# Kernel optimization log

Hardware: AMD Instinct MI355X
Metric: run time of the kernel (lower is better)

## Reference

```python
import jax, jax.numpy as jnp
import numpy as np
from jax import lax

V = 25          # skeleton joints
GAMMA = 9       # temporal kernel size
PAD = (GAMMA - 1) // 2
# (C_in, C_out, temporal_stride) for the 10 SpatialTemporalConv blocks
CHANNELS = [(3, 64, 1), (64, 64, 1), (64, 64, 1), (64, 64, 1),
            (64, 128, 2), (128, 128, 1), (128, 128, 1),
            (128, 256, 2), (256, 256, 1), (256, 256, 1)]


def setup_inputs() -> dict:
    key = jax.random.key(0)
    keys = jax.random.split(key, 1 + 2 * len(CHANNELS))
    N, T = 64, 300
    x = jax.random.normal(keys[0], (N, T, V, 3), jnp.float32)

    # Normalized adjacency (uni-labeling strategy): D^-1/2 (A + I) D^-1/2
    rng = np.random.default_rng(0)
    adj = (rng.random((V, V)) < 0.15).astype(np.float32)
    adj = np.maximum(adj, adj.T)
    adj = adj + np.eye(V, dtype=np.float32)
    dinv = 1.0 / np.sqrt(adj.sum(axis=1))
    A = jnp.asarray(dinv[:, None] * adj * dinv[None, :])

    inp = {"x": x, "A": A}
    for i, (cin, cout, _s) in enumerate(CHANNELS):
        inp[f"ws{i}"] = jax.random.normal(keys[1 + 2 * i], (cout, cin), jnp.float32) * np.float32(np.sqrt(2.0 / (cin * V)))
        inp[f"wt{i}"] = jax.random.normal(keys[2 + 2 * i], (cout, cout, GAMMA), jnp.float32) * np.float32(np.sqrt(2.0 / (cout * GAMMA)))
    return inp


def _st_block(f, A, ws, wt, stride):
    """One SpatialTemporalConv: 1x1 spatial GCN (channel mix + adjacency matmul),
    ReLU, then (gamma x 1) temporal conv with given stride, ReLU.
    f: (N, C_in, T, V) -> (N, C_out, T//stride, V)"""
    g = jnp.einsum('nctv,oc->notv', f, ws)       # 1x1 conv channel mixing
    g = jnp.einsum('nctv,vw->nctw', g, A)        # graph adjacency multiply
    g = jax.nn.relu(g)
    out = lax.conv_general_dilated(
        g, wt[:, :, :, None],                    # (O, I, gamma, 1)
        window_strides=(stride, 1),
        padding=((PAD, PAD), (0, 0)),
        dimension_numbers=('NCHW', 'OIHW', 'NCHW'))
    return jax.nn.relu(out)


def reference(x, A, ws0, ws1, ws2, ws3, ws4, ws5, ws6, ws7, ws8, ws9,
              wt0, wt1, wt2, wt3, wt4, wt5, wt6, wt7, wt8, wt9):
    ws = [ws0, ws1, ws2, ws3, ws4, ws5, ws6, ws7, ws8, ws9]
    wt = [wt0, wt1, wt2, wt3, wt4, wt5, wt6, wt7, wt8, wt9]
    f = jnp.transpose(x, (0, 3, 1, 2))  # (N,T,V,C) -> (N,C,T,V)
    for i, (_cin, _cout, s) in enumerate(CHANNELS):
        f = _st_block(f, A, ws[i], wt[i], s)
    return f  # (N, 256, T//4, V)
```

## Files before the change

### kernel.cpp

```cpp
#include <hip/hip_runtime.h>
#include <cstdint>

typedef unsigned short u16;
typedef unsigned int u32;
typedef __attribute__((ext_vector_type(8))) short short8v;
typedef __attribute__((ext_vector_type(4))) float float4v;

#define MFMA16 __builtin_amdgcn_mfma_f32_16x16x32_bf16

__device__ __forceinline__ u16 f2bf(float x) {
    union { float f; u32 u; } c; c.f = x;
    return (u16)((c.u + 0x7FFFu + ((c.u >> 16) & 1u)) >> 16);
}
__device__ __forceinline__ float bf2f(u16 h) {
    union { u32 u; float f; } c; c.u = ((u32)h) << 16;
    return c.f;
}

__device__ __forceinline__ void dma16(const void* g, void* l) {
    __builtin_amdgcn_global_load_lds(
        (const __attribute__((address_space(1))) u32*)g,
        (__attribute__((address_space(3))) u32*)l, 16, 0, 0);
}

__global__ void zinit(u32* p) { p[threadIdx.x] = 0u; }

__global__ __launch_bounds__(256)
void prep_w(const float* __restrict__ W, u16* __restrict__ dst,
            int M, int cin, int nIC, int TAPS, int total)
{
    int e = blockIdx.x * 256 + threadIdx.x;
    if (e >= total) return;
    int tmp = e;
    int j = tmp & 7; tmp >>= 3;
    int m = tmp % M; tmp /= M;
    int kg = tmp & 3; tmp >>= 2;
    int p = tmp & 1; tmp >>= 1;
    int ic = tmp % nIC;
    int tap = tmp / nIC;
    int i = ic * 32 + kg * 8 + j;
    float val = (i < cin) ? W[((size_t)m * cin + i) * TAPS + tap] : 0.f;
    u16 h = f2bf(val);
    dst[e] = p ? f2bf(val - bf2f(h)) : h;
}

__global__ __launch_bounds__(256)
void adj0(const float* __restrict__ x, const float* __restrict__ Am,
          u16* __restrict__ dstb, long dst_nstride, int dst_poff)
{
    __shared__ float A_s[25][26];
    for (int i2 = threadIdx.x; i2 < 625; i2 += 256) A_s[i2 / 25][i2 % 25] = Am[i2];
    __syncthreads();
    int t = blockIdx.x * 256 + threadIdx.x;
    int nl = blockIdx.y;
    if (t >= 300) return;
    const float* xp = x + ((size_t)nl * 300 + t) * 75;
    float acc[25][3];
#pragma unroll
    for (int w = 0; w < 25; ++w) { acc[w][0] = 0.f; acc[w][1] = 0.f; acc[w][2] = 0.f; }
    for (int v = 0; v < 25; ++v) {
        float x0 = xp[v * 3 + 0], x1 = xp[v * 3 + 1], x2 = xp[v * 3 + 2];
#pragma unroll
        for (int w = 0; w < 25; ++w) {
            float a = A_s[v][w];
            acc[w][0] = fmaf(a, x0, acc[w][0]);
            acc[w][1] = fmaf(a, x1, acc[w][1]);
            acc[w][2] = fmaf(a, x2, acc[w][2]);
        }
    }
    u16* dhi = dstb + (size_t)nl * dst_nstride;
    u16* dlo = dhi + dst_poff;
#pragma unroll
    for (int w = 0; w < 25; ++w) {
        u16 hb[32], lb[32];
#pragma unroll
        for (int c = 0; c < 32; ++c) { hb[c] = 0; lb[c] = 0; }
#pragma unroll
        for (int c = 0; c < 3; ++c) {
            float y = acc[w][c];
            u16 h = f2bf(y);
            hb[c] = h; lb[c] = f2bf(y - bf2f(h));
        }
        size_t o = ((size_t)w * 300 + t) * 32;
#pragma unroll
        for (int q = 0; q < 4; ++q) {
            *(uint4*)&dhi[o + q * 8] = *(const uint4*)&hb[q * 8];
            *(uint4*)&dlo[o + q * 8] = *(const uint4*)&lb[q * 8];
        }
    }
}

__global__ __launch_bounds__(256)
void adj_ip(u16* fb, const float* __restrict__ Am, int C, int Tin,
            long nstride, int poff)
{
    __shared__ float A_s[25][26];
    for (int i2 = threadIdx.x; i2 < 625; i2 += 256) A_s[i2 / 25][i2 % 25] = Am[i2];
    __syncthreads();
    const int C4 = C >> 2;
    int idx = blockIdx.x * 256 + threadIdx.x;
    if (idx >= Tin * C4) return;
    int t = idx / C4;
    int c = (idx - t * C4) * 4;
    u16* hi = fb + (size_t)blockIdx.y * nstride;
    u16* lo = hi + poff;
    float a0[25], a1[25], a2[25], a3[25];
#pragma unroll
    for (int w = 0; w < 25; ++w) { a0[w] = 0.f; a1[w] = 0.f; a2[w] = 0.f; a3[w] = 0.f; }
    for (int v = 0; v < 25; ++v) {
        size_t o = (size_t)(v * Tin + t) * C + c;
        ushort4 h4 = *(const ushort4*)&hi[o];
        ushort4 l4 = *(const ushort4*)&lo[o];
        float y0 = bf2f(h4.x) + bf2f(l4.x);
        float y1 = bf2f(h4.y) + bf2f(l4.y);
        float y2 = bf2f(h4.z) + bf2f(l4.z);
        float y3 = bf2f(h4.w) + bf2f(l4.w);
#pragma unroll
        for (int w = 0; w < 25; ++w) {
            float a = A_s[v][w];
            a0[w] = fmaf(a, y0, a0[w]);
            a1[w] = fmaf(a, y1, a1[w]);
            a2[w] = fmaf(a, y2, a2[w]);
            a3[w] = fmaf(a, y3, a3[w]);
        }
    }
#pragma unroll
    for (int w = 0; w < 25; ++w) {
        size_t o = (size_t)(w * Tin + t) * C + c;
        ushort4 ho, lo4; u16 h;
        h = f2bf(a0[w]); ho.x = h; lo4.x = f2bf(a0[w] - bf2f(h));
        h = f2bf(a1[w]); ho.y = h; lo4.y = f2bf(a1[w] - bf2f(h));
        h = f2bf(a2[w]); ho.z = h; lo4.z = f2bf(a2[w] - bf2f(h));
        h = f2bf(a3[w]); ho.w = h; lo4.w = f2bf(a3[w] - bf2f(h));
        *(ushort4*)&hi[o] = ho;
        *(ushort4*)&lo[o] = lo4;
    }
}

template<int VW, int NT, int TAPS, int S, int OUTF32, int MINW>
__global__ __launch_bounds__(256, MINW)
void conv8(const u16* __restrict__ srcb, const u16* __restrict__ wtp,
           u16* __restrict__ dstb, float* __restrict__ outb,
           int K, int M, int Tin, int Tout,
           long src_nstride, int src_poff, long dst_nstride, int dst_poff,
           int o_tiles, int strips, int cnt, const u16* __restrict__ zpage)
{
    constexpr int PADW = (TAPS == 1) ? 0 : 4;
    constexpr int NPH = (S == 2) ? 2 : 1;
    constexpr int RAW = (TAPS == 1) ? NT : ((S == 1) ? NT + 8 : NT + 4);
    constexpr int RQ = 32 / (VW * NPH);
    constexpr int R = ((RAW + RQ - 1) / RQ) * RQ;
    constexpr int NF = NT / 16;
    constexpr int NB = (VW * 2 * NPH * R * 4) / 256;
    static_assert((VW * 2 * NPH * R * 4) % 256 == 0, "chunk mult");
    constexpr int BUF_U16 = VW * 2 * NPH * R * 32;
    constexpr int PL_STRIDE = NPH * R * 32;
    constexpr int EP = (VW == 2) ? 34 : 18;
    constexpr int SMEM_B = 2 * BUF_U16 * 2;
    static_assert(VW * NT * EP * 4 <= SMEM_B, "E fits");
    static_assert(SMEM_B <= 65536, "LDS limit");
    constexpr bool PING = (NF <= 4);
    constexpr int NVG = (VW == 4) ? 7 : 13;
    __shared__ __align__(16) char smem[SMEM_B];
    u16* Bs = (u16*)smem;
    float* E = (float*)smem;

    const int tid = threadIdx.x;
    const int l15 = tid & 15;
    const int lkg = (tid >> 4) & 3;
    const int wv = tid >> 6;
    const int vh = (VW == 2) ? (wv >> 1) : wv;
    const int oh = (VW == 2) ? (wv & 1) : 0;

    int Wk;
    {
        const int nwg = gridDim.x;
        int q8 = nwg >> 3, r8 = nwg & 7;
        int xcd = blockIdx.x & 7, bl = blockIdx.x >> 3;
        Wk = (xcd < r8 ? xcd * (q8 + 1) : r8 * (q8 + 1) + (xcd - r8) * q8) + bl;
    }
    const int vg = Wk % NVG; int r0 = Wk / NVG;
    const int strip = r0 % strips; r0 /= strips;
    const int nl = r0 % cnt;
    const int ot = r0 / cnt;

    const int t0 = strip * NT;
    const int wstart = t0 * S - PADW;
    const int nIC = K >> 5;
    const int obase = (VW == 2) ? (ot * 128 + oh * 64 + l15) : (ot * 64 + l15);

    const u16* shi = srcb + (size_t)nl * src_nstride;
    const u16* slo = shi + src_poff;

    float4v acc[4][NF];
#pragma unroll
    for (int mt = 0; mt < 4; ++mt)
#pragma unroll
        for (int nf = 0; nf < NF; ++nf) acc[mt][nf] = (float4v)0.f;

    const char* bptr[NB];
#pragma unroll
    for (int k = 0; k < NB; ++k) {
        int d = k * 256 + tid;
        int part = d & 3; int d2 = d >> 2;
        int rw = d2 % R; d2 /= R;
        int ph = (NPH == 2) ? (d2 % NPH) : 0; d2 /= NPH;
        int pl = d2 & 1; int w2 = d2 >> 1;
        int v = vg * VW + w2;
        int t = (S == 2) ? (wstart + 2 * rw + ph) : (wstart + rw);
        int psrc = (part - (rw >> 1)) & 3;
        bool ok = (v < 25) && (t >= 0) && (t < Tin);
        const u16* base = pl ? slo : shi;
        bptr[k] = ok ? (const char*)(base + ((size_t)(v * Tin + t) * K + psrc * 8))
                     : (const char*)zpage;
    }

    auto stage = [&](int buf, int ic) {
        u16* base = Bs + buf * BUF_U16 + (tid & 192) * 8;
#pragma unroll
        for (int k = 0; k < NB; ++k)
            dma16(bptr[k] + (size_t)ic * 64, base + k * 2048);
    };
    auto prefA = [&](uint4(&a)[8], int tap, int ic) {
        const u16* base = wtp + (size_t)(tap * nIC + ic) * (64 * M);
#pragma unroll
        for (int pl = 0; pl < 2; ++pl)
#pragma unroll
            for (int mt = 0; mt < 4; ++mt)
                a[pl * 4 + mt] = *(const uint4*)(base + ((size_t)(pl * 4 + lkg) * M + obase + mt * 16) * 8);
    };
    auto ctap = [&](const uint4(&a)[8], int tap, int buf) {
        const u16* bb0 = Bs + buf * BUF_U16;
#pragma unroll
        for (int nf = 0; nf < NF; ++nf) {
            const int tt = nf * 16 + l15;
            const int rw = (S == 2) ? (tt + (tap >> 1)) : (tt + tap);
            const int ph = (S == 2) ? (tap & 1) : 0;
            const int sl = (lkg + (rw >> 1)) & 3;
            const u16* p = bb0 + (size_t)(((vh * 2 * NPH + ph) * R + rw) * 4 + sl) * 8;
            short8v bh = *(const short8v*)p;
            short8v bl = *(const short8v*)(p + PL_STRIDE);
#pragma unroll
            for (int mt = 0; mt < 4; ++mt) {
                short8v ah = __builtin_bit_cast(short8v, a[mt]);
                short8v al = __builtin_bit_cast(short8v, a[4 + mt]);
                acc[mt][nf] = MFMA16(ah, bh, acc[mt][nf], 0, 0, 0);
                acc[mt][nf] = MFMA16(ah, bl, acc[mt][nf], 0, 0, 0);
                acc[mt][nf] = MFMA16(al, bh, acc[mt][nf], 0, 0, 0);
            }
        }
    };

    if constexpr (PING) {
        uint4 aA[8], aB[8];
        stage(0, 0);
        prefA(aA, 0, 0);
        __syncthreads();
        int cur = 0;
#pragma unroll 1
        for (int ic = 0; ic < nIC; ++ic) {
            const int icn = (ic + 1 < nIC) ? ic + 1 : ic;
            if (ic + 1 < nIC) stage(cur ^ 1, ic + 1);
#pragma unroll
            for (int t = 0; t < TAPS; ++t) {
                const int tn = (t + 1 < TAPS) ? t + 1 : 0;
                const int ici = (t + 1 < TAPS) ? ic : icn;
                if ((t & 1) == 0) { prefA(aB, tn, ici); ctap(aA, t, cur); }
                else              { prefA(aA, tn, ici); ctap(aB, t, cur); }
            }
            if ((TAPS & 1) != 0) {
#pragma unroll
                for (int j = 0; j < 8; ++j) aA[j] = aB[j];
            }
            __syncthreads();
            cur ^= 1;
        }
    } else {
        stage(0, 0);
        __syncthreads();
        int cur = 0;
#pragma unroll 1
        for (int ic = 0; ic < nIC; ++ic) {
            if (ic + 1 < nIC) stage(cur ^ 1, ic + 1);
#pragma unroll
            for (int t = 0; t < TAPS; ++t) {
                uint4 a[8];
                prefA(a, t, ic);
                ctap(a, t, cur);
            }
            __syncthreads();
            cur ^= 1;
        }
    }

    u16* dhi = dstb ? dstb + (size_t)nl * dst_nstride : nullptr;
    u16* dlo = dhi ? dhi + dst_poff : nullptr;
    float* outn = OUTF32 ? outb + (size_t)nl * 480000 : nullptr;
#pragma unroll
    for (int m = 0; m < 4; ++m) {
        __syncthreads();
#pragma unroll
        for (int nf = 0; nf < NF; ++nf)
#pragma unroll
            for (int r = 0; r < 4; ++r)
                E[(vh * NT + nf * 16 + l15) * EP + ((VW == 2) ? oh * 16 : 0) + lkg * 4 + r] = acc[m][nf][r];
        __syncthreads();
        if (!OUTF32) {
            constexpr int C16 = (VW == 2) ? 2 : 1;
            for (int q = tid; q < VW * NT * C16; q += 256) {
                int row = q / C16, c16 = q - row * C16;
                int vv = vg * VW + row / NT;
                int tl = row % NT, tg = t0 + tl;
                if (vv < 25 && tg < Tout) {
                    u16 hb[16], lb[16];
#pragma unroll
                    for (int j = 0; j < 16; ++j) {
                        float y = fmaxf(E[row * EP + c16 * 16 + j], 0.f);
                        u16 h = f2bf(y); hb[j] = h; lb[j] = f2bf(y - bf2f(h));
                    }
                    int ob = ot * (VW == 2 ? 128 : 64) + c16 * 64 + m * 16;
                    size_t o = (size_t)(vv * Tout + tg) * M + ob;
                    *(uint4*)&dhi[o] = *(const uint4*)&hb[0];
                    *(uint4*)&dhi[o + 8] = *(const uint4*)&hb[8];
                    *(uint4*)&dlo[o] = *(const uint4*)&lb[0];
                    *(uint4*)&dlo[o + 8] = *(const uint4*)&lb[8];
                }
            }
        } else {
            for (int q = tid; q < 32 * NT; q += 256) {
                int ol = q / NT, tl = q - ol * NT, tg = t0 + tl;
                if (tg < Tout) {
                    int o = ot * 128 + (ol >> 4) * 64 + m * 16 + (ol & 15);
                    float* op = outn + (size_t)o * 1875 + tg * 25 + vg * 2;
#pragma unroll
                    for (int v2 = 0; v2 < 2; ++v2)
                        if (vg * 2 + v2 < 25)
                            op[v2] = fmaxf(E[(v2 * NT + tl) * EP + ol], 0.f);
                }
            }
        }
    }
}

extern "C" void kernel_launch(void* const* d_in, const int* in_sizes, int n_in,
                              void* d_out, int out_size, void* d_ws, size_t ws_size,
                              hipStream_t stream)
{
    const float* x = (const float*)d_in[0];
    const float* A = (const float*)d_in[1];
    const float* WS[10];
    const float* WT[10];
    for (int i = 0; i < 10; ++i) {
        WS[i] = (const float*)d_in[2 + 2 * i];
        WT[i] = (const float*)d_in[3 + 2 * i];
    }
    float* outF = (float*)d_out;

    static const int KM[10]  = {32, 64, 64, 64, 64, 128, 128, 128, 256, 256};
    static const int MM[10]  = {64, 64, 64, 64, 128, 128, 128, 256, 256, 256};
    static const int TIN[10] = {300, 300, 300, 300, 300, 150, 150, 150, 75, 75};
    static const int SS[10]  = {1, 1, 1, 1, 2, 1, 1, 2, 1, 1};

    const u16* zpage = (const u16*)d_ws;
    zinit<<<1, 256, 0, stream>>>((u32*)d_ws);

    size_t mixoff[10], wtoff[10], off = 0;
    for (int b = 0; b < 10; ++b) {
        mixoff[b] = off; off += (size_t)(KM[b] / 32) * 64 * MM[b];
        wtoff[b] = off;  off += (size_t)9 * (MM[b] / 32) * 64 * MM[b];
    }
    u16* prep = (u16*)((char*)d_ws + 1024);
    size_t prep_bytes = ((off * 2 + 255) / 256) * 256;
    u16* ws_s = (u16*)((char*)d_ws + 1024 + prep_bytes);
    size_t ws_spill = (ws_size > prep_bytes + 1024) ? ws_size - prep_bytes - 1024 : 0;

    for (int b = 0; b < 10; ++b) {
        int nICm = KM[b] / 32;
        int totm = nICm * 64 * MM[b];
        prep_w<<<(totm + 255) / 256, 256, 0, stream>>>(
            WS[b], prep + mixoff[b], MM[b], (b == 0 ? 3 : KM[b]), nICm, 1, totm);
        int nICt = MM[b] / 32;
        int tott = 9 * nICt * 64 * MM[b];
        prep_w<<<(tott + 255) / 256, 256, 0, stream>>>(
            WT[b], prep + wtoff[b], MM[b], MM[b], nICt, 9, tott);
    }

    const long F_STR = 960000;
    const long S_STR = 1920000;
    const size_t F_PN_B = 1920000;
    const size_t S_PN_B = 3840000;
    const size_t dout_b = (size_t)out_size * 4;

    int done = 0;
    while (done < 64) {
        size_t used = (size_t)done * F_PN_B;
        size_t dout_rem = dout_b - used;
        int NC = (int)((dout_rem + ws_spill) / (F_PN_B + S_PN_B));
        if (NC > 64 - done) NC = 64 - done;
        if (NC < 1) NC = 1;
        int k_s = 0;
        for (;; --NC) {
            long rem_after_F = (long)dout_rem - (long)NC * (long)F_PN_B;
            k_s = rem_after_F > 0 ? (int)(rem_after_F / (long)S_PN_B) : 0;
            if (k_s > NC) k_s = NC;
            if ((size_t)(NC - k_s) * S_PN_B <= ws_spill) break;
            if (NC <= 1) { NC = 1; k_s = 0; break; }
        }
        u16* Fz = (u16*)d_out + used / 2;
        u16* Sd = (u16*)d_out + (used + (size_t)NC * F_PN_B) / 2;

        for (int b = 0; b < 10; ++b) {
            const int K = KM[b], M = MM[b], Tin = TIN[b], S = SS[b];
            const int Tout = (S == 1) ? Tin : Tin / 2;
            const int fpoff = (b == 0) ? 240000 : 480000;
            const int spoff = 25 * Tin * M;

            if (b == 0)
                adj0<<<dim3(2, NC), 256, 0, stream>>>(
                    x + (size_t)done * 22500, A, Fz, F_STR, 240000);
            else {
                int thr = Tin * (K >> 2);
                adj_ip<<<dim3((thr + 255) / 256, NC), 256, 0, stream>>>(
                    Fz, A, K, Tin, F_STR, 480000);
            }

            for (int part = 0; part < 2; ++part) {
                int n0 = part ? k_s : 0;
                int cnt = part ? NC - k_s : k_s;
                if (cnt <= 0) continue;
                u16* sb = part ? ws_s : Sd;
                u16* fb = Fz + (size_t)n0 * F_STR;

                if (b <= 3) {
                    const int otm = 1, strips = 5;
                    conv8<4, 64, 1, 1, 0, 2><<<otm * 7 * strips * cnt, 256, 0, stream>>>(
                        fb, prep + mixoff[b], sb, nullptr, K, M, Tin, Tin,
                        F_STR, fpoff, S_STR, spoff, otm, strips, cnt, zpage);
                } else {
                    const int otm = M / 128, strips = (Tin + 79) / 80;
                    conv8<2, 80, 1, 1, 0, 2><<<otm * 13 * strips * cnt, 256, 0, stream>>>(
                        fb, prep + mixoff[b], sb, nullptr, K, M, Tin, Tin,
                        F_STR, fpoff, S_STR, spoff, otm, strips, cnt, zpage);
                }

                if (b <= 3) {
                    const int ott = 1, strips = (Tin + 47) / 48;
                    conv8<4, 48, 9, 1, 0, 2><<<ott * 7 * strips * cnt, 256, 0, stream>>>(
                        sb, prep + wtoff[b], fb, nullptr, M, M, Tin, Tout,
                        S_STR, spoff, F_STR, 480000, ott, strips, cnt, zpage);
                } else if (S == 2) {
                    const int ott = M / 128, strips = (Tout + 47) / 48;
                    conv8<2, 48, 9, 2, 0, 2><<<ott * 13 * strips * cnt, 256, 0, stream>>>(
                        sb, prep + wtoff[b], fb, nullptr, M, M, Tin, Tout,
                        S_STR, spoff, F_STR, 480000, ott, strips, cnt, zpage);
                } else if (b == 9) {
                    const int ott = 2, strips = 1;
                    conv8<2, 80, 9, 1, 1, 3><<<ott * 13 * strips * cnt, 256, 0, stream>>>(
                        sb, prep + wtoff[b], nullptr,
                        outF + (size_t)(done + n0) * 480000,
                        M, M, Tin, Tout, S_STR, spoff, 0, 0, ott, strips, cnt, zpage);
                } else {
                    const int ott = M / 128, strips = (Tout + 79) / 80;
                    conv8<2, 80, 9, 1, 0, 3><<<ott * 13 * strips * cnt, 256, 0, stream>>>(
                        sb, prep + wtoff[b], fb, nullptr, M, M, Tin, Tout,
                        S_STR, spoff, F_STR, 480000, ott, strips, cnt, zpage);
                }
            }
        }
        done += NC;
    }
}
```

Baseline: 4.337 ms.

## Prefetch hi weight plane across taps and reorder workgroup index decomposition

For the non-ping path (more than 4 fragments), the hi weight plane for the next tap is now double-buffered in registers while the lo plane is loaded just in time, and the MFMA loop is split into a hi pass and a lo pass. The workgroup decomposition is reordered so output tiles vary fastest, then batch, strip and vertex group, which changes which blocks share operands in L2. Launch bounds are unified to a minimum of 2 waves per SIMD, lowering the occupancy hint from 3 for the 80-wide stride-1 temporal convs. This aims to hide weight-load latency and improve cache locality, at the cost of more register pressure, a second LDS read pass, and possibly lower occupancy.

```diff
diff --git a/kernel.cpp b/kernel.cpp
--- a/kernel.cpp
+++ b/kernel.cpp
@@ -137,13 +137,13 @@
     }
 }
 
-template<int VW, int NT, int TAPS, int S, int OUTF32, int MINW>
-__global__ __launch_bounds__(256, MINW)
-void conv8(const u16* __restrict__ srcb, const u16* __restrict__ wtp,
-           u16* __restrict__ dstb, float* __restrict__ outb,
-           int K, int M, int Tin, int Tout,
-           long src_nstride, int src_poff, long dst_nstride, int dst_poff,
-           int o_tiles, int strips, int cnt, const u16* __restrict__ zpage)
+template<int VW, int NT, int TAPS, int S, int OUTF32>
+__global__ __launch_bounds__(256, 2)
+void conv10(const u16* __restrict__ srcb, const u16* __restrict__ wtp,
+            u16* __restrict__ dstb, float* __restrict__ outb,
+            int K, int M, int Tin, int Tout,
+            long src_nstride, int src_poff, long dst_nstride, int dst_poff,
+            int o_tiles, int strips, int cnt, const u16* __restrict__ zpage)
 {
     constexpr int PADW = (TAPS == 1) ? 0 : 4;
     constexpr int NPH = (S == 2) ? 2 : 1;
@@ -179,10 +179,10 @@
         int xcd = blockIdx.x & 7, bl = blockIdx.x >> 3;
         Wk = (xcd < r8 ? xcd * (q8 + 1) : r8 * (q8 + 1) + (xcd - r8) * q8) + bl;
     }
-    const int vg = Wk % NVG; int r0 = Wk / NVG;
-    const int strip = r0 % strips; r0 /= strips;
-    const int nl = r0 % cnt;
-    const int ot = r0 / cnt;
+    const int ot = Wk % o_tiles; int r0 = Wk / o_tiles;
+    const int nl = r0 % cnt; r0 /= cnt;
+    const int strip = r0 % strips;
+    const int vg = r0 / strips;
 
     const int t0 = strip * NT;
     const int wstart = t0 * S - PADW;
@@ -229,6 +229,18 @@
             for (int mt = 0; mt < 4; ++mt)
                 a[pl * 4 + mt] = *(const uint4*)(base + ((size_t)(pl * 4 + lkg) * M + obase + mt * 16) * 8);
     };
+    auto prefH = [&](uint4(&a)[4], int tap, int ic) {
+        const u16* base = wtp + (size_t)(tap * nIC + ic) * (64 * M);
+#pragma unroll
+        for (int mt = 0; mt < 4; ++mt)
+            a[mt] = *(const uint4*)(base + ((size_t)lkg * M + obase + mt * 16) * 8);
+    };
+    auto prefL = [&](uint4(&a)[4], int tap, int ic) {
+        const u16* base = wtp + (size_t)(tap * nIC + ic) * (64 * M);
+#pragma unroll
+        for (int mt = 0; mt < 4; ++mt)
+            a[mt] = *(const uint4*)(base + ((size_t)(4 + lkg) * M + obase + mt * 16) * 8);
+    };
     auto ctap = [&](const uint4(&a)[8], int tap, int buf) {
         const u16* bb0 = Bs + buf * BUF_U16;
 #pragma unroll
@@ -247,6 +259,39 @@
                 acc[mt][nf] = MFMA16(ah, bh, acc[mt][nf], 0, 0, 0);
                 acc[mt][nf] = MFMA16(ah, bl, acc[mt][nf], 0, 0, 0);
                 acc[mt][nf] = MFMA16(al, bh, acc[mt][nf], 0, 0, 0);
+            }
+        }
+    };
+    auto ctapHL = [&](const uint4(&ah)[4], const uint4(&al)[4], int tap, int buf) {
+        const u16* bb0 = Bs + buf * BUF_U16;
+#pragma unroll
+        for (int nf = 0; nf < NF; ++nf) {
+            const int tt = nf * 16 + l15;
+            const int rw = (S == 2) ? (tt + (tap >> 1)) : (tt + tap);
+            const int ph = (S == 2) ? (tap & 1) : 0;
+            const int sl = (lkg + (rw >> 1)) & 3;
+            const u16* p = bb0 + (size_t)(((vh * 2 * NPH + ph) * R + rw) * 4 + sl) * 8;
+            short8v bh = *(const short8v*)p;
+            short8v bl = *(const short8v*)(p + PL_STRIDE);
+#pragma unroll
+            for (int mt = 0; mt < 4; ++mt) {
+                short8v a = __builtin_bit_cast(short8v, ah[mt]);
+                acc[mt][nf] = MFMA16(a, bh, acc[mt][nf], 0, 0, 0);
+                acc[mt][nf] = MFMA16(a, bl, acc[mt][nf], 0, 0, 0);
+            }
+        }
+#pragma unroll
+        for (int nf = 0; nf < NF; ++nf) {
+            const int tt = nf * 16 + l15;
+            const int rw = (S == 2) ? (tt + (tap >> 1)) : (tt + tap);
+            const int ph = (S == 2) ? (tap & 1) : 0;
+            const int sl = (lkg + (rw >> 1)) & 3;
+            const u16* p = bb0 + (size_t)(((vh * 2 * NPH + ph) * R + rw) * 4 + sl) * 8;
+            short8v bh = *(const short8v*)p;
+#pragma unroll
+            for (int mt = 0; mt < 4; ++mt) {
+                short8v a = __builtin_bit_cast(short8v, al[mt]);
+                acc[mt][nf] = MFMA16(a, bh, acc[mt][nf], 0, 0, 0);
             }
         }
     };
@@ -276,17 +321,25 @@
             cur ^= 1;
         }
     } else {
+        uint4 hA[4], hB[4], al[4];
         stage(0, 0);
+        prefH(hA, 0, 0);
         __syncthreads();
         int cur = 0;
 #pragma unroll 1
         for (int ic = 0; ic < nIC; ++ic) {
+            const int icn = (ic + 1 < nIC) ? ic + 1 : ic;
             if (ic + 1 < nIC) stage(cur ^ 1, ic + 1);
 #pragma unroll
             for (int t = 0; t < TAPS; ++t) {
-                uint4 a[8];
-                prefA(a, t, ic);
-                ctap(a, t, cur);
+                const int tn = (t + 1 < TAPS) ? t + 1 : 0;
+                const int ici = (t + 1 < TAPS) ? ic : icn;
+                if ((t & 1) == 0) { prefH(hB, tn, ici); prefL(al, t, ic); ctapHL(hA, al, t, cur); }
+                else              { prefH(hA, tn, ici); prefL(al, t, ic); ctapHL(hB, al, t, cur); }
+            }
+            if ((TAPS & 1) != 0) {
+#pragma unroll
+                for (int j = 0; j < 4; ++j) hA[j] = hB[j];
             }
             __syncthreads();
             cur ^= 1;
@@ -433,35 +486,35 @@
 
                 if (b <= 3) {
                     const int otm = 1, strips = 5;
-                    conv8<4, 64, 1, 1, 0, 2><<<otm * 7 * strips * cnt, 256, 0, stream>>>(
+                    conv10<4, 64, 1, 1, 0><<<otm * 7 * strips * cnt, 256, 0, stream>>>(
                         fb, prep + mixoff[b], sb, nullptr, K, M, Tin, Tin,
                         F_STR, fpoff, S_STR, spoff, otm, strips, cnt, zpage);
                 } else {
                     const int otm = M / 128, strips = (Tin + 79) / 80;
-                    conv8<2, 80, 1, 1, 0, 2><<<otm * 13 * strips * cnt, 256, 0, stream>>>(
+                    conv10<2, 80, 1, 1, 0><<<otm * 13 * strips * cnt, 256, 0, stream>>>(
                         fb, prep + mixoff[b], sb, nullptr, K, M, Tin, Tin,
                         F_STR, fpoff, S_STR, spoff, otm, strips, cnt, zpage);
                 }
 
                 if (b <= 3) {
                     const int ott = 1, strips = (Tin + 47) / 48;
-                    conv8<4, 48, 9, 1, 0, 2><<<ott * 7 * strips * cnt, 256, 0, stream>>>(
+                    conv10<4, 48, 9, 1, 0><<<ott * 7 * strips * cnt, 256, 0, stream>>>(
                         sb, prep + wtoff[b], fb, nullptr, M, M, Tin, Tout,
                         S_STR, spoff, F_STR, 480000, ott, strips, cnt, zpage);
                 } else if (S == 2) {
                     const int ott = M / 128, strips = (Tout + 47) / 48;
-                    conv8<2, 48, 9, 2, 0, 2><<<ott * 13 * strips * cnt, 256, 0, stream>>>(
+                    conv10<2, 48, 9, 2, 0><<<ott * 13 * strips * cnt, 256, 0, stream>>>(
                         sb, prep + wtoff[b], fb, nullptr, M, M, Tin, Tout,
                         S_STR, spoff, F_STR, 480000, ott, strips, cnt, zpage);
                 } else if (b == 9) {
                     const int ott = 2, strips = 1;
-                    conv8<2, 80, 9, 1, 1, 3><<<ott * 13 * strips * cnt, 256, 0, stream>>>(
+                    conv10<2, 80, 9, 1, 1><<<ott * 13 * strips * cnt, 256, 0, stream>>>(
                         sb, prep + wtoff[b], nullptr,
                         outF + (size_t)(done + n0) * 480000,
                         M, M, Tin, Tout, S_STR, spoff, 0, 0, ott, strips, cnt, zpage);
                 } else {
                     const int ott = M / 128, strips = (Tout + 79) / 80;
-                    conv8<2, 80, 9, 1, 0, 3><<<ott * 13 * strips * cnt, 256, 0, stream>>>(
+                    conv10<2, 80, 9, 1, 0><<<ott * 13 * strips * cnt, 256, 0, stream>>>(
                         sb, prep + wtoff[b], fb, nullptr, M, M, Tin, Tout,
                         S_STR, spoff, F_STR, 480000, ott, strips, cnt, zpage);
                 }
```

After: 4.196 ms. 1.03x faster.
